# Kernel tuning notes

Measured on AMD Instinct MI355X. Metric: run time of the kernel, lower is better.

## Reference

```python
import jax, jax.numpy as jnp
import numpy as np

N = 100000      # nodes
E = 800000      # directed edges per branch
HID = 128
FOUT = 128
HEADS = 2
LAYERS = 3      # convlayer
JK_LAYERS = 3
H2 = (JK_LAYERS * HID) // 2   # PyG JK-LSTM hidden size = 192
N_AA = 26
N_SS = 3


def setup_inputs() -> dict:
    key = jax.random.key(0)
    ks = iter(jax.random.split(key, 32))
    def nrm(shape, scale=0.05):
        return jax.random.normal(next(ks), shape, dtype=jnp.float32) * scale
    return {
        "x_idx": jax.random.randint(next(ks), (N, 2), 0, N_SS),
        "x_flt": jax.random.normal(next(ks), (N, 5), dtype=jnp.float32),
        "edge_index_l": jax.random.randint(next(ks), (2, E), 0, N),
        "edge_index_r": jax.random.randint(next(ks), (2, E), 0, N),
        "emb_aa": nrm((2, N_AA, HID - 5)),          # [branch, vocab, hid-5]
        "emb_ss": nrm((2, N_SS, HID - 5)),
        "conv_W": nrm((2, LAYERS, HID, HEADS * HID)),
        "conv_att_src": nrm((2, LAYERS, HEADS, HID)),
        "conv_att_dst": nrm((2, LAYERS, HEADS, HID)),
        "conv_bias": nrm((2, LAYERS, HID)),
        "lstm_Wih": nrm((2, 2, 4 * H2, HID)),        # [branch, direction, 4H2, hid]
        "lstm_Whh": nrm((2, 2, 4 * H2, H2)),
        "lstm_bih": nrm((2, 2, 4 * H2)),
        "lstm_bhh": nrm((2, 2, 4 * H2)),
        "jk_att_W": nrm((2, 2 * H2)),
        "jk_att_b": nrm((2,)),
        "dummy_W": nrm((2, HID, HID)),
        "dummy_b": nrm((2, HID)),
        "fin_W": nrm((4, HID, FOUT)),
        "fin_b": nrm((4, FOUT)),
        "last_W": nrm((FOUT,)),                      # Linear(fout,1,bias=False)
    }


def _gat_conv(x, src, dst, W, att_src, att_dst, bias):
    # PyG GATConv, concat=False (mean over heads), leaky_relu slope 0.2
    n = x.shape[0]
    h, c = att_src.shape
    xh = (x @ W).reshape(n, h, c)                         # [N,H,C]
    a_src = jnp.einsum('nhc,hc->nh', xh, att_src)
    a_dst = jnp.einsum('nhc,hc->nh', xh, att_dst)
    e = jax.nn.leaky_relu(a_src[src] + a_dst[dst], 0.2)   # [E,H]
    m = jax.ops.segment_max(e, dst, num_segments=n)
    ex = jnp.exp(e - m[dst])
    denom = jax.ops.segment_sum(ex, dst, num_segments=n)
    alpha = ex / (denom[dst] + 1e-16)                     # segment softmax over dst
    out = jax.ops.segment_sum(xh[src] * alpha[:, :, None], dst, num_segments=n)
    return out.mean(axis=1) + bias                        # [N,C]


def _lstm_dir(xs, Wih, Whh, bih, bhh, reverse):
    # xs: [L,N,C]; single-layer LSTM, torch gate order i,f,g,o
    n = xs.shape[1]
    h2 = Whh.shape[1]
    b = bih + bhh
    def cell(carry, xt):
        h, c = carry
        g = xt @ Wih.T + h @ Whh.T + b
        i, f, gg, o = jnp.split(g, 4, axis=-1)
        c = jax.nn.sigmoid(f) * c + jax.nn.sigmoid(i) * jnp.tanh(gg)
        h = jax.nn.sigmoid(o) * jnp.tanh(c)
        return (h, c), h
    init = (jnp.zeros((n, h2), xs.dtype), jnp.zeros((n, h2), xs.dtype))
    _, hs = jax.lax.scan(cell, init, xs, reverse=reverse)
    return hs  # [L,N,H2]


def _jk(xs, Wih, Whh, bih, bhh, att_w, att_b):
    # PyG JumpingKnowledge('lstm'): bi-LSTM over layer axis + scalar attention
    hf = _lstm_dir(xs, Wih[0], Whh[0], bih[0], bhh[0], False)
    hb = _lstm_dir(xs, Wih[1], Whh[1], bih[1], bhh[1], True)
    h = jnp.concatenate([hf, hb], axis=-1)                # [L,N,2H2]
    a = jax.nn.softmax(jnp.einsum('lnh,h->ln', h, att_w) + att_b, axis=0)
    return (xs * a[..., None]).sum(axis=0)                # [N,C]


def _forward(x_idx, x_flt, edge_index_l, edge_index_r, emb_aa, emb_ss,
             conv_W, conv_att_src, conv_att_dst, conv_bias,
             lstm_Wih, lstm_Whh, lstm_bih, lstm_bhh, jk_att_W, jk_att_b,
             dummy_W, dummy_b, fin_W, fin_b, last_W):
    n = x_idx.shape[0]
    loops = jnp.arange(n)  # GATConv add_self_loops=True
    src_l = jnp.concatenate([edge_index_l[0], loops]); dst_l = jnp.concatenate([edge_index_l[1], loops])
    src_r = jnp.concatenate([edge_index_r[0], loops]); dst_r = jnp.concatenate([edge_index_r[1], loops])
    x_l = jnp.concatenate([emb_aa[0][x_idx[:, 0]] + emb_ss[0][x_idx[:, 1]], x_flt], axis=1)
    x_r = jnp.concatenate([emb_aa[1][x_idx[:, 0]] + emb_ss[1][x_idx[:, 1]], x_flt], axis=1)
    xs_l, xs_r = [], []
    for i in range(LAYERS):
        mean = (x_l + x_r) * 0.5
        o_l = mean + jax.nn.relu(_gat_conv(x_l, src_l, dst_l, conv_W[0, i], conv_att_src[0, i], conv_att_dst[0, i], conv_bias[0, i]))
        o_r = mean + jax.nn.relu(_gat_conv(x_r, src_r, dst_r, conv_W[1, i], conv_att_src[1, i], conv_att_dst[1, i], conv_bias[1, i]))
        x_l, x_r = o_l, o_r
        xs_l.append(x_l); xs_r.append(x_r)
    jk_l = _jk(jnp.stack(xs_l), lstm_Wih[0], lstm_Whh[0], lstm_bih[0], lstm_bhh[0], jk_att_W[0], jk_att_b[0])
    jk_r = _jk(jnp.stack(xs_r), lstm_Wih[1], lstm_Whh[1], lstm_bih[1], lstm_bhh[1], jk_att_W[1], jk_att_b[1])
    sq_l = jk_l @ dummy_W[0] + dummy_b[0]
    sq_r = jk_r @ dummy_W[1] + dummy_b[1]
    feats = [jk_l, sq_l, jk_r, sq_r]
    outs = [feats[i] @ fin_W[i] + fin_b[i] for i in range(4)]
    alpha = jax.nn.softmax(jnp.stack([o @ last_W for o in outs], axis=1), axis=1)  # [N,4]
    nodeemb = sum(outs[i] * alpha[:, i:i + 1] for i in range(4))
    return nodeemb


def reference(x_idx, x_flt, edge_index_l, edge_index_r, emb_aa, emb_ss,
              conv_W, conv_att_src, conv_att_dst, conv_bias,
              lstm_Wih, lstm_Whh, lstm_bih, lstm_bhh, jk_att_W, jk_att_b,
              dummy_W, dummy_b, fin_W, fin_b, last_W):
    return _forward(x_idx, x_flt, edge_index_l, edge_index_r, emb_aa, emb_ss,
                    conv_W, conv_att_src, conv_att_dst, conv_bias,
                    lstm_Wih, lstm_Whh, lstm_bih, lstm_bhh, jk_att_W, jk_att_b,
                    dummy_W, dummy_b, fin_W, fin_b, last_W)
```

## Files before the change

### kernel.cpp

```cpp
#include <hip/hip_runtime.h>
#include <cstddef>
#include <cstdint>

#define N_NODES 100000
#define N_EDGES 800000
#define EL_TOT  900000
#define HID 128
#define H2  192
#define G4  768
#define CH3 50000
#define BK  32
#define LDST 32
#define SCANB 98

typedef unsigned short bf16;
typedef __attribute__((ext_vector_type(8))) short bf16x8v;
typedef __attribute__((ext_vector_type(4))) float f32x4v;

#define AS1 __attribute__((address_space(1)))
#define AS3 __attribute__((address_space(3)))

__device__ __forceinline__ void async16(const bf16* g, bf16* l) {
    __builtin_amdgcn_global_load_lds((AS1 void*)g, (AS3 void*)l, 16, 0, 0);
}


__device__ __forceinline__ float b2f(bf16 u) {
    return __uint_as_float(((unsigned)u) << 16);
}
__device__ __forceinline__ bf16 f2b(float f) {
    unsigned u = __float_as_uint(f);
    u += 0x7FFFu + ((u >> 16) & 1u);
    return (bf16)(u >> 16);
}
__device__ __forceinline__ void stE(float* p, size_t i, float v) { p[i] = v; }
__device__ __forceinline__ void stE(bf16* p, size_t i, float v) { p[i] = f2b(v); }
__device__ __forceinline__ float ftanh(float x) {
    float cx = fminf(fmaxf(x, -15.f), 15.f);
    float e = __expf(2.f * cx);
    return (e - 1.f) / (e + 1.f);
}

__device__ __forceinline__ float x0_val(int c, int ia, int is_, int n,
                                        const float* __restrict__ embA,
                                        const float* __restrict__ embS,
                                        const float* __restrict__ xflt) {
    return (c < 123) ? (embA[ia * 123 + c] + embS[is_ * 123 + c])
                     : xflt[n * 5 + (c - 123)];
}

__device__ __forceinline__ int lstm_perm(int j) {
    int w = j & 63, tt = j >> 6;
    return (w >> 4) * 192 + tt * 16 + (w & 15);
}

__device__ __forceinline__ bool swz_tile(int R, int ntile, int& bm0, int& nt) {
    const int id = blockIdx.x;
    const int xcd = id & 7;
    const int s = id >> 3;
    nt = s % ntile;
    const int yp = (s / ntile) * 8 + xcd;
    if (yp * 128 >= R) return false;
    bm0 = yp * 128;
    return true;
}
static inline int swz_grid(int R, int ntile) {
    int panels = (R + 127) / 128;
    return 8 * ntile * ((panels + 7) / 8);
}


__global__ void sentinel_kernel(float* out, int n, float val) {
    int t = blockIdx.x * blockDim.x + threadIdx.x;
    if (t < n) out[t] = val;
}

__global__ void bsum_perm_kernel(const float* __restrict__ bih,
                                 const float* __restrict__ bhh,
                                 float* __restrict__ bsum) {
    int t = blockIdx.x * blockDim.x + threadIdx.x;
    if (t >= 4 * G4) return;
    int d = t / G4, j = t % G4;
    int orig = lstm_perm(j);
    bsum[t] = bih[d * G4 + orig] + bhh[d * G4 + orig];
}

__global__ void lstm_w_perm_kernel(const float* __restrict__ in,
                                   bf16* __restrict__ out, int K) {
    long long t = (long long)blockIdx.x * blockDim.x + threadIdx.x;
    long long tot = 4LL * G4 * K;
    if (t >= tot) return;
    int k = (int)(t % K);
    int j = (int)((t / K) % G4);
    int d = (int)(t / ((long long)G4 * K));
    int orig = lstm_perm(j);
    out[t] = f2b(in[((size_t)d * G4 + orig) * K + k]);
}

__global__ void trans_kernel(const float* __restrict__ in, bf16* __restrict__ out,
                             int batch, int K, int M) {
    long long t = (long long)blockIdx.x * blockDim.x + threadIdx.x;
    long long tot = (long long)batch * K * M;
    if (t >= tot) return;
    int per = K * M;
    int bt = (int)(t / per);
    int rem = (int)(t % per);
    int m = rem / K, k = rem % K;
    out[t] = f2b(in[(size_t)bt * per + (size_t)k * M + m]);
}


__global__ void deg_kernel(const int* __restrict__ dst, int* __restrict__ deg) {
    int t = blockIdx.x * blockDim.x + threadIdx.x;
    if (t >= EL_TOT) return;
    int d = (t < N_EDGES) ? dst[t] : (t - N_EDGES);
    atomicAdd(&deg[d], 1);
}

__global__ void scan1_kernel(const int* __restrict__ deg0, const int* __restrict__ deg1,
                             int* __restrict__ tmp0, int* __restrict__ tmp1,
                             int* __restrict__ bsums) {
    __shared__ int sdata[1024];
    const int b = blockIdx.y;
    const int* deg = b ? deg1 : deg0;
    int* tmp = b ? tmp1 : tmp0;
    int i = blockIdx.x * 1024 + threadIdx.x;
    int v = (i < N_NODES) ? deg[i] : 0;
    sdata[threadIdx.x] = v;
    __syncthreads();
    for (int off = 1; off < 1024; off <<= 1) {
        int t = (threadIdx.x >= (unsigned)off) ? sdata[threadIdx.x - off] : 0;
        __syncthreads();
        sdata[threadIdx.x] += t;
        __syncthreads();
    }
    if (i < N_NODES) tmp[i] = sdata[threadIdx.x];
    if (threadIdx.x == 1023) bsums[b * SCANB + blockIdx.x] = sdata[1023];
}

__global__ void scan2_kernel(int* __restrict__ bsums) {
    int b = threadIdx.x;
    if (b < 2) {
        int c = 0;
        for (int k = 0; k < SCANB; ++k) {
            int t = bsums[b * SCANB + k];
            bsums[b * SCANB + k] = c;
            c += t;
        }
    }
}

__global__ void scan3_kernel(const int* __restrict__ bsums,
                             const int* __restrict__ deg0, const int* __restrict__ deg1,
                             const int* __restrict__ tmp0, const int* __restrict__ tmp1,
                             int* __restrict__ offs0, int* __restrict__ offs1,
                             int* __restrict__ pos0, int* __restrict__ pos1) {
    const int b = blockIdx.y;
    const int* deg = b ? deg1 : deg0;
    const int* tmp = b ? tmp1 : tmp0;
    int* offs = b ? offs1 : offs0;
    int* pos = b ? pos1 : pos0;
    int carry = bsums[b * SCANB + blockIdx.x];
    int i = blockIdx.x * 1024 + threadIdx.x;
    if (i < N_NODES) {
        int inc = tmp[i] + carry;
        offs[i + 1] = inc;
        pos[i] = inc - deg[i];
    }
    if (i == 0) offs[0] = 0;
}

__global__ void fill_kernel(const int* __restrict__ srcrow,
                            const int* __restrict__ dstrow,
                            int* __restrict__ pos, int* __restrict__ srcs) {
    int t = blockIdx.x * blockDim.x + threadIdx.x;
    if (t >= EL_TOT) return;
    int s, d;
    if (t < N_EDGES) { s = srcrow[t]; d = dstrow[t]; }
    else             { s = d = t - N_EDGES; }
    int p = atomicAdd(&pos[d], 1);
    srcs[p] = s;
}

template<typename TC>
__device__ __forceinline__ void gemm128_body(
    const bf16* __restrict__ A1, const bf16* __restrict__ B1, int K1,
    TC* __restrict__ C, const float* __restrict__ bias, int R, int M,
    int bm0, int bn0) {
    __shared__ bf16 As[2][128 * LDST];
    __shared__ bf16 Bs[2][128 * LDST];
    const int tid = threadIdx.x;
    const int lane = tid & 63;
    const int wave = tid >> 6;
    const int wm = (wave & 1) * 64, wn = (wave >> 1) * 64;
    const int l15 = lane & 15;
    const int q8 = (lane >> 4) * 8;
    const int lr = lane >> 2;
    const int lc = (lane & 3) * 8;

    f32x4v acc[4][4];
#pragma unroll
    for (int i = 0; i < 4; ++i)
#pragma unroll
        for (int j = 0; j < 4; ++j) acc[i][j] = (f32x4v)(0.0f);

    const int ns = K1 / BK;
    auto stage = [&](int buf, int s) {
        const int k0 = s * BK;
#pragma unroll
        for (int rnd = 0; rnd < 2; ++rnd) {
            const int rbase = wave * 16 + rnd * 64;
            const int row = rbase + lr;
            int ga = bm0 + row; ga = (ga < R) ? ga : (R - 1);
            async16(A1 + (size_t)ga * K1 + k0 + lc, &As[buf][rbase * LDST]);
            async16(B1 + (size_t)(bn0 + row) * K1 + k0 + lc, &Bs[buf][rbase * LDST]);
        }
    };

    stage(0, 0);
    __syncthreads();
    for (int s = 0; s < ns; ++s) {
        const int cur = s & 1;
        if (s + 1 < ns) stage(cur ^ 1, s + 1);
        bf16x8v af[4], bfv[4];
#pragma unroll
        for (int i = 0; i < 4; ++i) {
            af[i]  = *(const bf16x8v*)&As[cur][(wm + i * 16 + l15) * LDST + q8];
            bfv[i] = *(const bf16x8v*)&Bs[cur][(wn + i * 16 + l15) * LDST + q8];
        }
#pragma unroll
        for (int i = 0; i < 4; ++i)
#pragma unroll
            for (int j = 0; j < 4; ++j)
                acc[i][j] = __builtin_amdgcn_mfma_f32_16x16x32_bf16(
                    af[i], bfv[j], acc[i][j], 0, 0, 0);
        __syncthreads();
    }

#pragma unroll
    for (int i = 0; i < 4; ++i) {
        const int row0 = bm0 + wm + i * 16 + (lane >> 4) * 4;
#pragma unroll
        for (int j = 0; j < 4; ++j) {
            const int col = bn0 + wn + j * 16 + l15;
            const float bv = bias ? bias[col] : 0.f;
#pragma unroll
            for (int r = 0; r < 4; ++r) {
                const int gr = row0 + r;
                if (gr < R) stE(C, (size_t)gr * M + col, acc[i][j][r] + bv);
            }
        }
    }
}

template<typename TC>
__global__ __launch_bounds__(256) void mfma_gemm_kernel(
    const bf16* __restrict__ A1, const bf16* __restrict__ B1, int K1,
    TC* __restrict__ C, const float* __restrict__ bias, int R, int M) {
    int bm0, nt;
    if (!swz_tile(R, M >> 7, bm0, nt)) return;
    gemm128_body<TC>(A1, B1, K1, C, bias, R, M, bm0, nt * 128);
}

template<typename TC>
__global__ __launch_bounds__(256) void mfma_gemm_b_kernel(
    const bf16* a0, const bf16* a1, const bf16* a2, const bf16* a3,
    const bf16* __restrict__ Bbase,
    TC* c0, TC* c1, TC* c2, TC* c3,
    const float* __restrict__ bias, int R) {
    int bm0, nt;
    if (!swz_tile(R, 1, bm0, nt)) return;
    const int y = blockIdx.y;
    const bf16* A1 = (y == 0) ? a0 : (y == 1) ? a1 : (y == 2) ? a2 : a3;
    TC* C = (y == 0) ? c0 : (y == 1) ? c1 : (y == 2) ? c2 : c3;
    gemm128_body<TC>(A1, Bbase + (size_t)y * 128 * 128, 128, C,
                     bias + (size_t)y * 128, R, 128, bm0, 0);
}

__global__ __launch_bounds__(256) void lstm_gemm_kernel(
    const bf16* __restrict__ A1, const bf16* __restrict__ B1,
    const bf16* __restrict__ A2, const bf16* __restrict__ B2,
    const float* __restrict__ bias, bf16* __restrict__ c_state,
    bf16* __restrict__ h_out, const float* __restrict__ aw,
    float* __restrict__ score, int first, int last, int R) {
    __shared__ bf16 As[2][128 * LDST];
    __shared__ bf16 Bs[2][128 * LDST];
    int bm0, nt;
    if (!swz_tile(R, G4 >> 7, bm0, nt)) return;
    const int bn0 = nt * 128;
    const int tid = threadIdx.x;
    const int lane = tid & 63;
    const int wave = tid >> 6;
    const int wm = (wave & 1) * 64, wn = (wave >> 1) * 64;
    const int l15 = lane & 15;
    const int q = lane >> 4;
    const int q8 = q * 8;
    const int lr = lane >> 2;
    const int lc = (lane & 3) * 8;

    f32x4v acc[4][4];
#pragma unroll
    for (int i = 0; i < 4; ++i)
#pragma unroll
        for (int j = 0; j < 4; ++j) acc[i][j] = (f32x4v)(0.0f);

    const int n1 = HID / BK;
    const int ns = n1 + (first ? 0 : (H2 / BK));

    auto stage = [&](int buf, int s) {
        const bf16* Ap; const bf16* Bp; int K, k0;
        if (s < n1) { Ap = A1; Bp = B1; K = HID; k0 = s * BK; }
        else        { Ap = A2; Bp = B2; K = H2;  k0 = (s - n1) * BK; }
#pragma unroll
        for (int rnd = 0; rnd < 2; ++rnd) {
            const int rbase = wave * 16 + rnd * 64;
            const int row = rbase + lr;
            int ga = bm0 + row; ga = (ga < R) ? ga : (R - 1);
            async16(Ap + (size_t)ga * K + k0 + lc, &As[buf][rbase * LDST]);
            async16(Bp + (size_t)(bn0 + row) * K + k0 + lc, &Bs[buf][rbase * LDST]);
        }
    };

    stage(0, 0);
    __syncthreads();
    for (int s = 0; s < ns; ++s) {
        const int cur = s & 1;
        if (s + 1 < ns) stage(cur ^ 1, s + 1);
        bf16x8v af[4], bfv[4];
#pragma unroll
        for (int i = 0; i < 4; ++i) {
            af[i]  = *(const bf16x8v*)&As[cur][(wm + i * 16 + l15) * LDST + q8];
            bfv[i] = *(const bf16x8v*)&Bs[cur][(wn + i * 16 + l15) * LDST + q8];
        }
#pragma unroll
        for (int i = 0; i < 4; ++i)
#pragma unroll
            for (int j = 0; j < 4; ++j)
                acc[i][j] = __builtin_amdgcn_mfma_f32_16x16x32_bf16(
                    af[i], bfv[j], acc[i][j], 0, 0, 0);
        __syncthreads();
    }

    const int u = ((bn0 + wn) >> 6) * 16 + l15;
    const float awu = aw[u];
    float bv[4];
#pragma unroll
    for (int j = 0; j < 4; ++j) bv[j] = bias[bn0 + wn + j * 16 + l15];
    float psum[4][4];
#pragma unroll
    for (int i = 0; i < 4; ++i) {
        const int row0 = bm0 + wm + i * 16 + q * 4;
#pragma unroll
        for (int r = 0; r < 4; ++r) {
            const int gr = row0 + r;
            const bool ok = gr < R;
            float ig = acc[i][0][r] + bv[0];
            float fg = acc[i][1][r] + bv[1];
            float gg = acc[i][2][r] + bv[2];
            float og = acc[i][3][r] + bv[3];
            float si = 1.f / (1.f + __expf(-ig));
            float sf = 1.f / (1.f + __expf(-fg));
            float so = 1.f / (1.f + __expf(-og));
            float co = (ok && !first) ? b2f(c_state[(size_t)gr * H2 + u]) : 0.f;
            float cn = sf * co + si * ftanh(gg);
            float hn = so * ftanh(cn);
            if (ok && !last) {
                c_state[(size_t)gr * H2 + u] = f2b(cn);
                h_out[(size_t)gr * H2 + u] = f2b(hn);
            }
            psum[i][r] = hn * awu;
        }
    }
#pragma unroll
    for (int m = 1; m < 16; m <<= 1)
#pragma unroll
        for (int i = 0; i < 4; ++i)
#pragma unroll
            for (int r = 0; r < 4; ++r)
                psum[i][r] += __shfl_xor(psum[i][r], m);
    if (l15 == 0) {
#pragma unroll
        for (int i = 0; i < 4; ++i)
#pragma unroll
            for (int r = 0; r < 4; ++r) {
                const int gr = bm0 + wm + i * 16 + q * 4 + r;
                if (gr < R) atomicAdd(&score[gr], psum[i][r]);
            }
    }
}

__global__ __launch_bounds__(256) void mfma_gemm_x0_kernel(
    const int* __restrict__ xidx, const float* __restrict__ xflt,
    const float* __restrict__ embA, const float* __restrict__ embS,
    const bf16* __restrict__ B1, bf16* __restrict__ C, int R, int M) {
    __shared__ bf16 As[128 * LDST];
    __shared__ bf16 Bs[128 * LDST];
    int bm0, nt;
    if (!swz_tile(R, M >> 7, bm0, nt)) return;
    const int bn0 = nt * 128;
    const int tid = threadIdx.x;
    const int lane = tid & 63;
    const int wave = tid >> 6;
    const int wm = (wave & 1) * 64, wn = (wave >> 1) * 64;
    const int l15 = lane & 15;
    const int q8 = (lane >> 4) * 8;
    const int srow = tid >> 2;
    const int scol = (tid & 3) * 8;
    const int lr = lane >> 2;
    const int lc = (lane & 3) * 8;

    f32x4v acc[4][4];
#pragma unroll
    for (int i = 0; i < 4; ++i)
#pragma unroll
        for (int j = 0; j < 4; ++j) acc[i][j] = (f32x4v)(0.0f);

    for (int k0 = 0; k0 < 128; k0 += BK) {
#pragma unroll
        for (int rnd = 0; rnd < 2; ++rnd) {
            {
                int row = srow + rnd * 64;
                int ga = bm0 + row; ga = (ga < R) ? ga : (R - 1);
                int ia = xidx[2 * ga], is_ = xidx[2 * ga + 1];
                bf16 tmp[8];
#pragma unroll
                for (int t = 0; t < 8; ++t)
                    tmp[t] = f2b(x0_val(k0 + scol + t, ia, is_, ga, embA, embS, xflt));
                *(int4*)&As[row * LDST + scol] = *(const int4*)tmp;
            }
            {
                const int rbase = wave * 16 + rnd * 64;
                int row = rbase + lr;
                async16(B1 + (size_t)(bn0 + row) * 128 + k0 + lc, &Bs[rbase * LDST]);
            }
        }
        __syncthreads();
        bf16x8v af[4], bfv[4];
#pragma unroll
        for (int i = 0; i < 4; ++i) {
            af[i]  = *(const bf16x8v*)&As[(wm + i * 16 + l15) * LDST + q8];
            bfv[i] = *(const bf16x8v*)&Bs[(wn + i * 16 + l15) * LDST + q8];
        }
#pragma unroll
        for (int i = 0; i < 4; ++i)
#pragma unroll
            for (int j = 0; j < 4; ++j)
                acc[i][j] = __builtin_amdgcn_mfma_f32_16x16x32_bf16(
                    af[i], bfv[j], acc[i][j], 0, 0, 0);
        __syncthreads();
    }
#pragma unroll
    for (int i = 0; i < 4; ++i) {
        const int row0 = bm0 + wm + i * 16 + (lane >> 4) * 4;
#pragma unroll
        for (int j = 0; j < 4; ++j) {
            const int col = bn0 + wn + j * 16 + l15;
#pragma unroll
            for (int r = 0; r < 4; ++r) {
                const int gr = row0 + r;
                if (gr < R) C[(size_t)gr * M + col] = f2b(acc[i][j][r]);
            }
        }
    }
}


__global__ __launch_bounds__(256) void att_kernel(
    const bf16* __restrict__ xh, const float* __restrict__ as_,
    float* __restrict__ asrc) {
    int w = (blockIdx.x * blockDim.x + threadIdx.x) >> 6;
    int lane = threadIdx.x & 63;
    if (w >= N_NODES) return;
    const bf16* row = xh + (size_t)w * 256;
    float x0 = b2f(row[lane]), x1 = b2f(row[64 + lane]);
    float x2 = b2f(row[128 + lane]), x3 = b2f(row[192 + lane]);
    float s0 = x0 * as_[lane] + x1 * as_[64 + lane];
    float s1 = x2 * as_[128 + lane] + x3 * as_[192 + lane];
    for (int o = 1; o < 64; o <<= 1) {
        s0 += __shfl_xor(s0, o); s1 += __shfl_xor(s1, o);
    }
    if (lane == 0) {
        asrc[2 * w] = s0; asrc[2 * w + 1] = s1;
    }
}

__device__ __forceinline__ float lrelu02(float x) { return x > 0.f ? x : 0.2f * x; }

__global__ __launch_bounds__(256) void agg_kernel(
    const bf16* __restrict__ xh, const float* __restrict__ asrc,
    const float* __restrict__ ad_, const int* __restrict__ offs,
    const int* __restrict__ srcs,
    const bf16* __restrict__ xprev_l, const bf16* __restrict__ xprev_r,
    const int* __restrict__ xidx, const float* __restrict__ xflt,
    const float* __restrict__ embAl, const float* __restrict__ embSl,
    const float* __restrict__ embAr, const float* __restrict__ embSr,
    const float* __restrict__ bias, bf16* __restrict__ outx) {
    int n = (blockIdx.x * blockDim.x + threadIdx.x) >> 6;
    int lane = threadIdx.x & 63;
    if (n >= N_NODES) return;
    const int start = offs[n], end = offs[n + 1];
    const int l15 = lane & 15;
    const int g = lane >> 4;

    float d0, d1;
    {
        uint2 v = *(const uint2*)(xh + (size_t)n * 256 + lane * 4);
        float p = ad_[lane * 4 + 0] * b2f((bf16)(v.x & 0xffffu))
                + ad_[lane * 4 + 1] * b2f((bf16)(v.x >> 16))
                + ad_[lane * 4 + 2] * b2f((bf16)(v.y & 0xffffu))
                + ad_[lane * 4 + 3] * b2f((bf16)(v.y >> 16));
        for (int o = 1; o < 32; o <<= 1) p += __shfl_xor(p, o);
        d0 = __shfl(p, 0);
        d1 = __shfl(p, 32);
    }

    float acc0[8] = {0, 0, 0, 0, 0, 0, 0, 0};
    float acc1[8] = {0, 0, 0, 0, 0, 0, 0, 0};
    float ds0 = 0.f, ds1 = 0.f;
#pragma unroll 2
    for (int j = start; j < end; j += 4) {
        int e = j + g;
        if (e < end) {
            int s = srcs[e];
            float2 a2 = *(const float2*)(asrc + 2 * s);
            float al0 = __expf(lrelu02(a2.x + d0));
            float al1 = __expf(lrelu02(a2.y + d1));
            if (l15 == 0) { ds0 += al0; ds1 += al1; }
            const bf16* row = xh + (size_t)s * 256 + l15 * 8;
            int4 v0 = *(const int4*)row;
            int4 v1 = *(const int4*)(row + 128);
            const int* w0 = (const int*)&v0;
            const int* w1 = (const int*)&v1;
#pragma unroll
            for (int t = 0; t < 4; ++t) {
                acc0[2 * t]     += __uint_as_float(((unsigned)w0[t]) << 16) * al0;
                acc0[2 * t + 1] += __uint_as_float(((unsigned)w0[t]) & 0xffff0000u) * al0;
                acc1[2 * t]     += __uint_as_float(((unsigned)w1[t]) << 16) * al1;
                acc1[2 * t + 1] += __uint_as_float(((unsigned)w1[t]) & 0xffff0000u) * al1;
            }
        }
    }
#pragma unroll
    for (int t = 0; t < 8; ++t) {
        acc0[t] += __shfl_xor(acc0[t], 16); acc0[t] += __shfl_xor(acc0[t], 32);
        acc1[t] += __shfl_xor(acc1[t], 16); acc1[t] += __shfl_xor(acc1[t], 32);
    }
    ds0 += __shfl_xor(ds0, 16); ds0 += __shfl_xor(ds0, 32);
    ds1 += __shfl_xor(ds1, 16); ds1 += __shfl_xor(ds1, 32);
    ds0 = __shfl(ds0, 0); ds1 = __shfl(ds1, 0);
    const float inv0 = 1.f / (ds0 + 1e-16f);
    const float inv1 = 1.f / (ds1 + 1e-16f);
    float accm[8];
#pragma unroll
    for (int t = 0; t < 8; ++t)
        accm[t] = 0.5f * (acc0[t] * inv0 + acc1[t] * inv1);

    if (lane < 16) {
        const int c0 = l15 * 8;
        const size_t base = (size_t)n * HID + c0;
        float xm[8];
        if (xidx) {
            int ia = xidx[2 * n], is_ = xidx[2 * n + 1];
#pragma unroll
            for (int t = 0; t < 8; ++t)
                xm[t] = 0.5f * (x0_val(c0 + t, ia, is_, n, embAl, embSl, xflt) +
                                x0_val(c0 + t, ia, is_, n, embAr, embSr, xflt));
        } else {
            int4 vl = *(const int4*)(xprev_l + base);
            int4 vr = *(const int4*)(xprev_r + base);
            const int* wl = (const int*)&vl;
            const int* wr = (const int*)&vr;
#pragma unroll
            for (int t = 0; t < 4; ++t) {
                xm[2 * t] = 0.5f * (__uint_as_float(((unsigned)wl[t]) << 16) +
                                    __uint_as_float(((unsigned)wr[t]) << 16));
                xm[2 * t + 1] = 0.5f * (__uint_as_float(((unsigned)wl[t]) & 0xffff0000u) +
                                        __uint_as_float(((unsigned)wr[t]) & 0xffff0000u));
            }
        }
        bf16 res[8];
#pragma unroll
        for (int t = 0; t < 8; ++t)
            res[t] = f2b(xm[t] + fmaxf(0.f, accm[t] + bias[c0 + t]));
        *(int4*)(outx + base) = *(const int4*)res;
    }
}


__global__ __launch_bounds__(256) void jkfin_kernel(
    const float* __restrict__ sb, const bf16* __restrict__ xs0,
    const bf16* __restrict__ xs1, const bf16* __restrict__ xs2,
    bf16* __restrict__ jk) {
    int w = (blockIdx.x * blockDim.x + threadIdx.x) >> 6;
    int lane = threadIdx.x & 63;
    if (w >= N_NODES) return;
    float s0 = sb[w], s1 = sb[N_NODES + w], s2 = sb[2 * N_NODES + w];
    float m = fmaxf(s0, fmaxf(s1, s2));
    float a0 = __expf(s0 - m), a1 = __expf(s1 - m), a2 = __expf(s2 - m);
    float inv = 1.f / (a0 + a1 + a2);
    a0 *= inv; a1 *= inv; a2 *= inv;
    size_t gn = (size_t)w * HID + lane * 2;
#pragma unroll
    for (int t = 0; t < 2; ++t) {
        float v0 = b2f(xs0[gn + t]);
        float v1 = b2f(xs1[gn + t]);
        float v2 = b2f(xs2[gn + t]);
        jk[gn + t] = f2b(v0 * a0 + v1 * a1 + v2 * a2);
    }
}

__global__ __launch_bounds__(256) void final_kernel(
    const float* __restrict__ o0, const float* __restrict__ o1,
    const float* __restrict__ o2, const float* __restrict__ o3,
    const float* __restrict__ lw, float* __restrict__ out, int nloc, long long c3off) {
    int w = (blockIdx.x * blockDim.x + threadIdx.x) >> 6;
    int lane = threadIdx.x & 63;
    if (w >= nloc) return;
    size_t base = (size_t)w * HID;
    float w0 = lw[lane], w1 = lw[64 + lane];
    const float* op[4] = {o0, o1, o2, o3};
    float v[4][2];
    float s[4];
#pragma unroll
    for (int i = 0; i < 4; ++i) {
        v[i][0] = op[i][base + lane];
        v[i][1] = op[i][base + 64 + lane];
        float t = v[i][0] * w0 + v[i][1] * w1;
        for (int o = 1; o < 64; o <<= 1) t += __shfl_xor(t, o);
        s[i] = t;
    }
    float m = fmaxf(fmaxf(s[0], s[1]), fmaxf(s[2], s[3]));
    float e0 = __expf(s[0] - m), e1 = __expf(s[1] - m);
    float e2 = __expf(s[2] - m), e3 = __expf(s[3] - m);
    float inv = 1.f / (e0 + e1 + e2 + e3);
    float r0 = (v[0][0] * e0 + v[1][0] * e1 + v[2][0] * e2 + v[3][0] * e3) * inv;
    float r1 = (v[0][1] * e0 + v[1][1] * e1 + v[2][1] * e2 + v[3][1] * e3) * inv;
    size_t obase = (size_t)(c3off + w) * HID;
    out[obase + lane] = r0;
    out[obase + 64 + lane] = r1;
}


static long long align1k(long long x) { return (x + 1023) & ~1023LL; }

extern "C" void kernel_launch(void* const* d_in, const int* in_sizes, int n_in,
                              void* d_out, int out_size, void* d_ws, size_t ws_size,
                              hipStream_t stream) {
    (void)in_sizes; (void)n_in; (void)out_size;
    const int*   x_idx   = (const int*)  d_in[0];
    const float* x_flt   = (const float*)d_in[1];
    const int*   ei_l    = (const int*)  d_in[2];
    const int*   ei_r    = (const int*)  d_in[3];
    const float* emb_aa  = (const float*)d_in[4];
    const float* emb_ss  = (const float*)d_in[5];
    const float* conv_W  = (const float*)d_in[6];
    const float* att_s   = (const float*)d_in[7];
    const float* att_d   = (const float*)d_in[8];
    const float* conv_b  = (const float*)d_in[9];
    const float* Wih     = (const float*)d_in[10];
    const float* Whh     = (const float*)d_in[11];
    const float* bih     = (const float*)d_in[12];
    const float* bhh     = (const float*)d_in[13];
    const float* jkw     = (const float*)d_in[14];
    const float* dummy_W = (const float*)d_in[16];
    const float* dummy_b = (const float*)d_in[17];
    const float* fin_W   = (const float*)d_in[18];
    const float* fin_b   = (const float*)d_in[19];
    const float* last_W  = (const float*)d_in[20];
    float* out = (float*)d_out;

    const long long S = (long long)N_NODES * HID;
    char* ws = (char*)d_ws;
    long long off = 0;

    bf16* hist = (bf16*)(ws + off);  off += align1k(6 * S * 2);
    float* scores = (float*)(ws + off); off += align1k(6LL * N_NODES * 4);
    float* bsum   = (float*)(ws + off); off += align1k(4LL * G4 * 4);
    int* bsums    = (int*)(ws + off);  off += align1k(2LL * SCANB * 4);
    bf16* Wih_b   = (bf16*)(ws + off); off += align1k(4LL * G4 * HID * 2);
    bf16* Whh_b   = (bf16*)(ws + off); off += align1k(4LL * G4 * H2 * 2);
    bf16* dummyWt = (bf16*)(ws + off); off += align1k(2LL * 128 * 128 * 2);
    bf16* finWt   = (bf16*)(ws + off); off += align1k(4LL * 128 * 128 * 2);

    char* BIG = ws + off;
    const long long slot0 = align1k(2 * S * 2);
    const long long slot1 = align1k((long long)N_NODES * H2 * 2);
    const long long need = off + slot0 + slot1;

    if ((long long)ws_size < need) {
        float val = 200000.0f + (float)(ws_size >> 20);
        sentinel_kernel<<<(N_NODES * HID + 255) / 256, 256, 0, stream>>>(
            out, N_NODES * HID, val);
        return;
    }

    bf16* xh  = (bf16*)BIG;
    bf16* jkb = (bf16*)BIG;
    int* ibase = (int*)(BIG + slot0);
    int *deg[2], *offs[2], *pos[2], *srcs[2];
    long long io = 0;
    for (int b = 0; b < 2; ++b) {
        deg[b]  = ibase + io; io += N_NODES;
        offs[b] = ibase + io; io += N_NODES + 1;
        pos[b]  = ibase + io; io += N_NODES;
        srcs[b] = ibase + io; io += EL_TOT;
    }
    long long io4a = ((io * 4 + 15) & ~15LL);
    float* asrc = (float*)(BIG + slot0 + io4a);
    bf16* convWt = (bf16*)(BIG + slot0 + io4a + 2LL * N_NODES * 4);
    bf16* hA = (bf16*)BIG;
    bf16* hB = (bf16*)d_out;
    bf16* cC = (bf16*)(BIG + slot0);

    const float* embA[2] = {emb_aa, emb_aa + 26 * 123};
    const float* embS[2] = {emb_ss, emb_ss + 3 * 123};

    bsum_perm_kernel<<<12, 256, 0, stream>>>(bih, bhh, bsum);
    trans_kernel<<<(6 * 128 * 256 + 255) / 256, 256, 0, stream>>>(
        conv_W, convWt, 6, 128, 256);
    lstm_w_perm_kernel<<<(4 * G4 * HID + 255) / 256, 256, 0, stream>>>(
        Wih, Wih_b, HID);
    lstm_w_perm_kernel<<<(4 * G4 * H2 + 255) / 256, 256, 0, stream>>>(
        Whh, Whh_b, H2);
    trans_kernel<<<(2 * 128 * 128 + 255) / 256, 256, 0, stream>>>(
        dummy_W, dummyWt, 2, 128, 128);
    trans_kernel<<<(4 * 128 * 128 + 255) / 256, 256, 0, stream>>>(
        fin_W, finWt, 4, 128, 128);
    hipMemsetAsync(deg[0], 0, N_NODES * sizeof(int), stream);
    hipMemsetAsync(deg[1], 0, N_NODES * sizeof(int), stream);
    deg_kernel<<<(EL_TOT + 255) / 256, 256, 0, stream>>>(ei_l + N_EDGES, deg[0]);
    deg_kernel<<<(EL_TOT + 255) / 256, 256, 0, stream>>>(ei_r + N_EDGES, deg[1]);
    scan1_kernel<<<dim3(SCANB, 2), 1024, 0, stream>>>(
        deg[0], deg[1], pos[0], pos[1], bsums);
    scan2_kernel<<<1, 64, 0, stream>>>(bsums);
    scan3_kernel<<<dim3(SCANB, 2), 1024, 0, stream>>>(
        bsums, deg[0], deg[1], pos[0], pos[1], offs[0], offs[1], pos[0], pos[1]);
    fill_kernel<<<(EL_TOT + 255) / 256, 256, 0, stream>>>(
        ei_l, ei_l + N_EDGES, pos[0], srcs[0]);
    fill_kernel<<<(EL_TOT + 255) / 256, 256, 0, stream>>>(
        ei_r, ei_r + N_EDGES, pos[1], srcs[1]);

    for (int i = 0; i < 3; ++i) {
        for (int b = 0; b < 2; ++b) {
            const bf16* Wc = convWt + (size_t)(b * 3 + i) * 256 * 128;
            if (i == 0) {
                mfma_gemm_x0_kernel<<<swz_grid(N_NODES, 2), 256, 0, stream>>>(
                    x_idx, x_flt, embA[b], embS[b], Wc, xh, N_NODES, 256);
            } else {
                mfma_gemm_kernel<bf16><<<swz_grid(N_NODES, 2), 256, 0, stream>>>(
                    hist + (size_t)(b * 3 + i - 1) * S, Wc, 128,
                    xh, nullptr, N_NODES, 256);
            }
            att_kernel<<<25000, 256, 0, stream>>>(
                xh, att_s + (size_t)(b * 3 + i) * 2 * HID, asrc);
            const bf16* xpl = (i == 0) ? nullptr : hist + (size_t)(i - 1) * S;
            const bf16* xpr = (i == 0) ? nullptr : hist + (size_t)(3 + i - 1) * S;
            agg_kernel<<<25000, 256, 0, stream>>>(
                xh, asrc, att_d + (size_t)(b * 3 + i) * 2 * HID,
                offs[b], srcs[b], xpl, xpr,
                (i == 0) ? x_idx : nullptr, x_flt,
                embA[0], embS[0], embA[1], embS[1],
                conv_b + (size_t)(b * 3 + i) * HID, hist + (size_t)(b * 3 + i) * S);
        }
    }

    hipMemsetAsync(scores, 0, (size_t)6 * N_NODES * 4, stream);
    const int gx = swz_grid(N_NODES, 6);
    for (int b = 0; b < 2; ++b) {
        for (int dir = 0; dir < 2; ++dir) {
            const int combo = b * 2 + dir;
            const bf16* Wi = Wih_b + (size_t)combo * G4 * HID;
            const bf16* Wh = Whh_b + (size_t)combo * G4 * H2;
            const float* bs = bsum + (size_t)combo * G4;
            const float* aw = jkw + (size_t)b * 2 * H2 + (size_t)dir * H2;
            for (int st = 0; st < 3; ++st) {
                int l = dir ? (2 - st) : st;
                const bf16* A = hist + (size_t)(b * 3 + l) * S;
                const bf16* hin = (st == 0) ? nullptr : ((st & 1) ? hA : hB);
                bf16* hout = (st & 1) ? hB : hA;
                lstm_gemm_kernel<<<gx, 256, 0, stream>>>(
                    A, Wi, hin, Wh, bs, cC, hout, aw,
                    scores + (size_t)(b * 3 + l) * N_NODES,
                    st == 0 ? 1 : 0, st == 2 ? 1 : 0, N_NODES);
            }
        }
    }
    for (int b = 0; b < 2; ++b)
        jkfin_kernel<<<25000, 256, 0, stream>>>(
            scores + (size_t)b * 3 * N_NODES,
            hist + (size_t)b * 3 * S, hist + (size_t)(b * 3 + 1) * S,
            hist + (size_t)(b * 3 + 2) * S, jkb + (size_t)b * S);

    float* f3 = (float*)hist;
    bf16* jkl = jkb; bf16* jkr = jkb + S;
    for (long long c3 = 0; c3 < N_NODES; c3 += CH3) {
        int Rr = (int)((N_NODES - c3) < CH3 ? (N_NODES - c3) : CH3);
        float* o0 = f3;
        float* o1 = f3 + 1LL * CH3 * HID;
        float* o2 = f3 + 2LL * CH3 * HID;
        float* o3 = f3 + 3LL * CH3 * HID;
        bf16* sql = (bf16*)(f3 + 4LL * CH3 * HID);
        bf16* sqr = sql + (long long)CH3 * HID;
        mfma_gemm_b_kernel<bf16><<<dim3(swz_grid(Rr, 1), 2), 256, 0, stream>>>(
            jkl + c3 * HID, jkr + c3 * HID, nullptr, nullptr,
            dummyWt, sql, sqr, nullptr, nullptr, dummy_b, Rr);
        mfma_gemm_b_kernel<float><<<dim3(swz_grid(Rr, 1), 4), 256, 0, stream>>>(
            jkl + c3 * HID, sql, jkr + c3 * HID, sqr,
            finWt, o0, o1, o2, o3, fin_b, Rr);
        final_kernel<<<(Rr + 3) / 4, 256, 0, stream>>>(
            o0, o1, o2, o3, last_W, out, Rr, c3);
    }
}
```

Before: 2.897 ms.

## Fuse source attention scores into conv GEMM epilogue and drop att_kernel

The per-node source attention logits are now computed inside the GEMM epilogue, from fp32 accumulators reduced across lanes and atomically added into a zeroed asrc buffer. This removes the separate att_kernel pass that re-read the whole xh matrix six times. Each call needs a memset plus atomics, and the logits are now taken from unrounded fp32 values instead of bf16. Separately, the aggregation loop unroll goes from 2 to 4 and every lane now accumulates the softmax denominator, which removes the lane-0 conditional and the final broadcast shuffle.

```diff
diff --git a/kernel.cpp b/kernel.cpp
--- a/kernel.cpp
+++ b/kernel.cpp
@@ -186,7 +186,7 @@
 __device__ __forceinline__ void gemm128_body(
     const bf16* __restrict__ A1, const bf16* __restrict__ B1, int K1,
     TC* __restrict__ C, const float* __restrict__ bias, int R, int M,
-    int bm0, int bn0) {
+    int bm0, int bn0, const float* __restrict__ as_, float* __restrict__ asrc) {
     __shared__ bf16 As[2][128 * LDST];
     __shared__ bf16 Bs[2][128 * LDST];
     const int tid = threadIdx.x;
@@ -237,9 +237,30 @@
         __syncthreads();
     }
 
+    const int head = bn0 >> 7;
 #pragma unroll
     for (int i = 0; i < 4; ++i) {
         const int row0 = bm0 + wm + i * 16 + (lane >> 4) * 4;
+        if (as_) {
+            float rs[4] = {0.f, 0.f, 0.f, 0.f};
+#pragma unroll
+            for (int j = 0; j < 4; ++j) {
+                const float w = as_[bn0 + wn + j * 16 + l15];
+#pragma unroll
+                for (int r = 0; r < 4; ++r) rs[r] += w * acc[i][j][r];
+            }
+#pragma unroll
+            for (int m = 1; m < 16; m <<= 1)
+#pragma unroll
+                for (int r = 0; r < 4; ++r) rs[r] += __shfl_xor(rs[r], m);
+            if (l15 == 0) {
+#pragma unroll
+                for (int r = 0; r < 4; ++r) {
+                    const int gr = row0 + r;
+                    if (gr < R) atomicAdd(&asrc[2 * gr + head], rs[r]);
+                }
+            }
+        }
 #pragma unroll
         for (int j = 0; j < 4; ++j) {
             const int col = bn0 + wn + j * 16 + l15;
@@ -256,10 +277,11 @@
 template<typename TC>
 __global__ __launch_bounds__(256) void mfma_gemm_kernel(
     const bf16* __restrict__ A1, const bf16* __restrict__ B1, int K1,
-    TC* __restrict__ C, const float* __restrict__ bias, int R, int M) {
+    TC* __restrict__ C, const float* __restrict__ bias, int R, int M,
+    const float* __restrict__ as_, float* __restrict__ asrc) {
     int bm0, nt;
     if (!swz_tile(R, M >> 7, bm0, nt)) return;
-    gemm128_body<TC>(A1, B1, K1, C, bias, R, M, bm0, nt * 128);
+    gemm128_body<TC>(A1, B1, K1, C, bias, R, M, bm0, nt * 128, as_, asrc);
 }
 
 template<typename TC>
@@ -274,7 +296,7 @@
     const bf16* A1 = (y == 0) ? a0 : (y == 1) ? a1 : (y == 2) ? a2 : a3;
     TC* C = (y == 0) ? c0 : (y == 1) ? c1 : (y == 2) ? c2 : c3;
     gemm128_body<TC>(A1, Bbase + (size_t)y * 128 * 128, 128, C,
-                     bias + (size_t)y * 128, R, 128, bm0, 0);
+                     bias + (size_t)y * 128, R, 128, bm0, 0, nullptr, nullptr);
 }
 
 __global__ __launch_bounds__(256) void lstm_gemm_kernel(
@@ -392,7 +414,8 @@
 __global__ __launch_bounds__(256) void mfma_gemm_x0_kernel(
     const int* __restrict__ xidx, const float* __restrict__ xflt,
     const float* __restrict__ embA, const float* __restrict__ embS,
-    const bf16* __restrict__ B1, bf16* __restrict__ C, int R, int M) {
+    const bf16* __restrict__ B1, bf16* __restrict__ C, int R, int M,
+    const float* __restrict__ as_, float* __restrict__ asrc) {
     __shared__ bf16 As[128 * LDST];
     __shared__ bf16 Bs[128 * LDST];
     int bm0, nt;
@@ -449,9 +472,30 @@
                     af[i], bfv[j], acc[i][j], 0, 0, 0);
         __syncthreads();
     }
+    const int head = bn0 >> 7;
 #pragma unroll
     for (int i = 0; i < 4; ++i) {
         const int row0 = bm0 + wm + i * 16 + (lane >> 4) * 4;
+        {
+            float rs[4] = {0.f, 0.f, 0.f, 0.f};
+#pragma unroll
+            for (int j = 0; j < 4; ++j) {
+                const float w = as_[bn0 + wn + j * 16 + l15];
+#pragma unroll
+                for (int r = 0; r < 4; ++r) rs[r] += w * acc[i][j][r];
+            }
+#pragma unroll
+            for (int m = 1; m < 16; m <<= 1)
+#pragma unroll
+                for (int r = 0; r < 4; ++r) rs[r] += __shfl_xor(rs[r], m);
+            if (l15 == 0) {
+#pragma unroll
+                for (int r = 0; r < 4; ++r) {
+                    const int gr = row0 + r;
+                    if (gr < R) atomicAdd(&asrc[2 * gr + head], rs[r]);
+                }
+            }
+        }
 #pragma unroll
         for (int j = 0; j < 4; ++j) {
             const int col = bn0 + wn + j * 16 + l15;
@@ -464,25 +508,6 @@
     }
 }
 
-
-__global__ __launch_bounds__(256) void att_kernel(
-    const bf16* __restrict__ xh, const float* __restrict__ as_,
-    float* __restrict__ asrc) {
-    int w = (blockIdx.x * blockDim.x + threadIdx.x) >> 6;
-    int lane = threadIdx.x & 63;
-    if (w >= N_NODES) return;
-    const bf16* row = xh + (size_t)w * 256;
-    float x0 = b2f(row[lane]), x1 = b2f(row[64 + lane]);
-    float x2 = b2f(row[128 + lane]), x3 = b2f(row[192 + lane]);
-    float s0 = x0 * as_[lane] + x1 * as_[64 + lane];
-    float s1 = x2 * as_[128 + lane] + x3 * as_[192 + lane];
-    for (int o = 1; o < 64; o <<= 1) {
-        s0 += __shfl_xor(s0, o); s1 += __shfl_xor(s1, o);
-    }
-    if (lane == 0) {
-        asrc[2 * w] = s0; asrc[2 * w + 1] = s1;
-    }
-}
 
 __device__ __forceinline__ float lrelu02(float x) { return x > 0.f ? x : 0.2f * x; }
 
@@ -517,7 +542,7 @@
     float acc0[8] = {0, 0, 0, 0, 0, 0, 0, 0};
     float acc1[8] = {0, 0, 0, 0, 0, 0, 0, 0};
     float ds0 = 0.f, ds1 = 0.f;
-#pragma unroll 2
+#pragma unroll 4
     for (int j = start; j < end; j += 4) {
         int e = j + g;
         if (e < end) {
@@ -525,7 +550,7 @@
             float2 a2 = *(const float2*)(asrc + 2 * s);
             float al0 = __expf(lrelu02(a2.x + d0));
             float al1 = __expf(lrelu02(a2.y + d1));
-            if (l15 == 0) { ds0 += al0; ds1 += al1; }
+            ds0 += al0; ds1 += al1;
             const bf16* row = xh + (size_t)s * 256 + l15 * 8;
             int4 v0 = *(const int4*)row;
             int4 v1 = *(const int4*)(row + 128);
@@ -547,7 +572,6 @@
     }
     ds0 += __shfl_xor(ds0, 16); ds0 += __shfl_xor(ds0, 32);
     ds1 += __shfl_xor(ds1, 16); ds1 += __shfl_xor(ds1, 32);
-    ds0 = __shfl(ds0, 0); ds1 = __shfl(ds1, 0);
     const float inv0 = 1.f / (ds0 + 1e-16f);
     const float inv1 = 1.f / (ds1 + 1e-16f);
     float accm[8];
@@ -743,16 +767,17 @@
     for (int i = 0; i < 3; ++i) {
         for (int b = 0; b < 2; ++b) {
             const bf16* Wc = convWt + (size_t)(b * 3 + i) * 256 * 128;
+            const float* as_ = att_s + (size_t)(b * 3 + i) * 2 * HID;
+            hipMemsetAsync(asrc, 0, 2LL * N_NODES * 4, stream);
             if (i == 0) {
                 mfma_gemm_x0_kernel<<<swz_grid(N_NODES, 2), 256, 0, stream>>>(
-                    x_idx, x_flt, embA[b], embS[b], Wc, xh, N_NODES, 256);
+                    x_idx, x_flt, embA[b], embS[b], Wc, xh, N_NODES, 256,
+                    as_, asrc);
             } else {
                 mfma_gemm_kernel<bf16><<<swz_grid(N_NODES, 2), 256, 0, stream>>>(
                     hist + (size_t)(b * 3 + i - 1) * S, Wc, 128,
-                    xh, nullptr, N_NODES, 256);
-            }
-            att_kernel<<<25000, 256, 0, stream>>>(
-                xh, att_s + (size_t)(b * 3 + i) * 2 * HID, asrc);
+                    xh, nullptr, N_NODES, 256, as_, asrc);
+            }
             const bf16* xpl = (i == 0) ? nullptr : hist + (size_t)(i - 1) * S;
             const bf16* xpr = (i == 0) ? nullptr : hist + (size_t)(3 + i - 1) * S;
             agg_kernel<<<25000, 256, 0, stream>>>(
```

Result: no change. 2.914 ms (+0.6%).
